# Kernel tuning notes

Measured on AMD Instinct MI355X. Metric: run time of the kernel, lower is better.

## Reference

```python
import jax, jax.numpy as jnp
import numpy as np

B, S, D, H = 1, 4096, 1024, 16
DH = D // H

def setup_inputs() -> dict:
    key = jax.random.key(0)
    ks = jax.random.split(key, 5)
    std = float(np.sqrt(2.0 / (D + D)))
    return {
        "x": jax.random.normal(ks[0], (B, S, D), dtype=jnp.float32),
        "Wq": jax.random.normal(ks[1], (D, D), dtype=jnp.float32) * std,
        "Wk": jax.random.normal(ks[2], (D, D), dtype=jnp.float32) * std,
        "Wv": jax.random.normal(ks[3], (D, D), dtype=jnp.float32) * std,
        "Wo": jax.random.normal(ks[4], (D, D), dtype=jnp.float32) * std,
    }

def reference(x, Wq, Wk, Wv, Wo):
    # projections: input @ W.T, then split heads: b s (h d) -> b h s d
    def split_heads(t):
        b, s, _ = t.shape
        return t.reshape(b, s, H, DH).transpose(0, 2, 1, 3)
    q = split_heads(x @ Wq.T)
    k = split_heads(x @ Wk.T)
    v = split_heads(x @ Wv.T)
    scale = 1.0 / jnp.sqrt(jnp.asarray(DH, dtype=x.dtype))
    scores = jnp.einsum("bhqd,bhkd->bhqk", q, k) * scale  # (b,h,s,s)
    # causal mask: allow k <= q
    causal = jnp.tril(jnp.ones((S, S), dtype=bool))
    scores = jnp.where(causal, scores, jnp.finfo(scores.dtype).min)
    attn = jax.nn.softmax(scores, axis=-1)
    out = jnp.einsum("bhqk,bhkd->bhqd", attn, v)  # (b,h,s,d)
    out = out.transpose(0, 2, 1, 3).reshape(B, S, D)  # b h s d -> b s (h d)
    return out @ Wo.T
```

## Files before the change

### kernel.cpp

```cpp
#include <hip/hip_runtime.h>
#include <math.h>

#define SEQ 4096
#define DM  1024
#define NH  16
#define DH  64

typedef _Float16 h16;
typedef __attribute__((ext_vector_type(4))) _Float16 h16x4;
typedef __attribute__((ext_vector_type(8))) _Float16 h16x8;
typedef __attribute__((ext_vector_type(4))) float f32x4;

__device__ __forceinline__ void gload_lds16(const h16* g, h16* l) {
    __builtin_amdgcn_global_load_lds(
        (const __attribute__((address_space(1))) void*)g,
        (__attribute__((address_space(3))) void*)l, 16, 0, 0);
}

__global__ __launch_bounds__(256) void cvt_all(const float* __restrict__ x,
                                               const float* __restrict__ wq,
                                               const float* __restrict__ wk,
                                               const float* __restrict__ wv,
                                               const float* __restrict__ wo,
                                               h16* __restrict__ dst) {
    const size_t SD4 = (size_t)SEQ * DM / 4;
    const size_t DD4 = (size_t)DM * DM / 4;
    const size_t i = (size_t)blockIdx.x * 256 + threadIdx.x;
    const float* src;
    size_t off;
    if (i < SD4) { src = x; off = i; }
    else {
        const size_t j = i - SD4;
        const int wsel = (int)(j >> 18);
        off = j & (DD4 - 1);
        src = (wsel == 0) ? wq : (wsel == 1) ? wk : (wsel == 2) ? wv : wo;
    }
    const float4 v = ((const float4*)src)[off];
    h16x4 o = { (h16)v.x, (h16)v.y, (h16)v.z, (h16)v.w };
    ((h16x4*)dst)[i] = o;
}

#define GT 32

__global__ __launch_bounds__(256) void gemm_qkv(const h16* __restrict__ xh,
                                                const h16* __restrict__ Wq,
                                                const h16* __restrict__ Wk,
                                                const h16* __restrict__ Wv,
                                                h16* __restrict__ Qh,
                                                h16* __restrict__ Kh,
                                                h16* __restrict__ Vth,
                                                float scl) {
    __shared__ h16 As[2][128 * GT];
    __shared__ h16 Bs[2][128 * GT];

    const int z    = blockIdx.z;
    const h16* B   = (z == 0) ? Wq : (z == 1) ? Wk : Wv;
    const int t    = threadIdx.x;
    const int lane = t & 63;
    const int w    = t >> 6;
    const int wm   = (w >> 1) * 64;
    const int wn   = (w & 1) * 64;
    const int l15  = lane & 15;
    const int lq   = lane >> 4;
    const int lq8  = lq * 8;
    const int m0   = blockIdx.y * 128;
    const int n0   = blockIdx.x * 128;
    const int K = DM, M = SEQ, N = DM;

    const int srow = w * 16 + (lane >> 2);
    const int scol = (lane & 3) * 8;
    const h16* pa0 = xh + (size_t)(m0 + srow) * K + scol;
    const h16* pa1 = xh + (size_t)(m0 + 64 + srow) * K + scol;
    const h16* pb0 = B  + (size_t)(n0 + srow) * K + scol;
    const h16* pb1 = B  + (size_t)(n0 + 64 + srow) * K + scol;

    f32x4 acc[4][4] = {};

    for (int k0 = 0; k0 < K; k0 += 64) {
        __syncthreads();
        #pragma unroll
        for (int s = 0; s < 2; ++s) {
            const int ko = k0 + s * 32;
            gload_lds16(pa0 + ko, &As[s][w * 512]);
            gload_lds16(pa1 + ko, &As[s][2048 + w * 512]);
            gload_lds16(pb0 + ko, &Bs[s][w * 512]);
            gload_lds16(pb1 + ko, &Bs[s][2048 + w * 512]);
        }
        __syncthreads();

        #pragma unroll
        for (int s = 0; s < 2; ++s) {
            h16x8 af[4], bf[4];
            #pragma unroll
            for (int i = 0; i < 4; ++i)
                af[i] = *(const h16x8*)&As[s][(wm + i * 16 + l15) * GT + lq8];
            #pragma unroll
            for (int j = 0; j < 4; ++j)
                bf[j] = *(const h16x8*)&Bs[s][(wn + j * 16 + l15) * GT + lq8];
            #pragma unroll
            for (int i = 0; i < 4; ++i)
                #pragma unroll
                for (int j = 0; j < 4; ++j)
                    acc[i][j] = __builtin_amdgcn_mfma_f32_16x16x32_f16(af[i], bf[j], acc[i][j], 0, 0, 0);
        }
    }

    const int cr = wm + lq * 4;
    const int cc = wn + l15;
    if (z == 2) {
        #pragma unroll
        for (int i = 0; i < 4; ++i)
            #pragma unroll
            for (int j = 0; j < 4; ++j) {
                const int gm0 = m0 + cr + i * 16;
                const int gn  = n0 + cc + j * 16;
                h16x4 v = { (h16)acc[i][j][0], (h16)acc[i][j][1],
                            (h16)acc[i][j][2], (h16)acc[i][j][3] };
                *(h16x4*)(Vth + (size_t)gn * M + gm0) = v;
            }
    } else {
        h16* Og = (z == 0) ? Qh : Kh;
        const float e = (z == 0) ? scl : 1.0f;
        #pragma unroll
        for (int i = 0; i < 4; ++i)
            #pragma unroll
            for (int j = 0; j < 4; ++j)
                #pragma unroll
                for (int r = 0; r < 4; ++r) {
                    const int gm = m0 + cr + i * 16 + r;
                    const int gn = n0 + cc + j * 16;
                    Og[(size_t)gm * N + gn] = (h16)(acc[i][j][r] * e);
                }
    }
}

__global__ __launch_bounds__(256) void gemm_out(const h16* __restrict__ A,
                                                const h16* __restrict__ B,
                                                float* __restrict__ C) {
    __shared__ h16 As[2][128 * GT];
    __shared__ h16 Bs[2][128 * GT];

    const int t    = threadIdx.x;
    const int lane = t & 63;
    const int w    = t >> 6;
    const int wm   = (w >> 1) * 64;
    const int wn   = (w & 1) * 64;
    const int l15  = lane & 15;
    const int lq   = lane >> 4;
    const int lq8  = lq * 8;
    const int m0   = blockIdx.y * 128;
    const int n0   = blockIdx.x * 128;
    const int K = DM, N = DM;

    const int srow = w * 16 + (lane >> 2);
    const int scol = (lane & 3) * 8;
    const h16* pa0 = A + (size_t)(m0 + srow) * K + scol;
    const h16* pa1 = A + (size_t)(m0 + 64 + srow) * K + scol;
    const h16* pb0 = B + (size_t)(n0 + srow) * K + scol;
    const h16* pb1 = B + (size_t)(n0 + 64 + srow) * K + scol;

    f32x4 acc[4][4] = {};

    for (int k0 = 0; k0 < K; k0 += 64) {
        __syncthreads();
        #pragma unroll
        for (int s = 0; s < 2; ++s) {
            const int ko = k0 + s * 32;
            gload_lds16(pa0 + ko, &As[s][w * 512]);
            gload_lds16(pa1 + ko, &As[s][2048 + w * 512]);
            gload_lds16(pb0 + ko, &Bs[s][w * 512]);
            gload_lds16(pb1 + ko, &Bs[s][2048 + w * 512]);
        }
        __syncthreads();

        #pragma unroll
        for (int s = 0; s < 2; ++s) {
            h16x8 af[4], bf[4];
            #pragma unroll
            for (int i = 0; i < 4; ++i)
                af[i] = *(const h16x8*)&As[s][(wm + i * 16 + l15) * GT + lq8];
            #pragma unroll
            for (int j = 0; j < 4; ++j)
                bf[j] = *(const h16x8*)&Bs[s][(wn + j * 16 + l15) * GT + lq8];
            #pragma unroll
            for (int i = 0; i < 4; ++i)
                #pragma unroll
                for (int j = 0; j < 4; ++j)
                    acc[i][j] = __builtin_amdgcn_mfma_f32_16x16x32_f16(af[i], bf[j], acc[i][j], 0, 0, 0);
        }
    }

    const int cr = wm + lq * 4;
    const int cc = wn + l15;
    #pragma unroll
    for (int i = 0; i < 4; ++i)
        #pragma unroll
        for (int j = 0; j < 4; ++j)
            #pragma unroll
            for (int r = 0; r < 4; ++r)
                C[(size_t)(m0 + cr + i * 16 + r) * N + n0 + cc + j * 16] = acc[i][j][r];
}

#define AST 80

__global__ __launch_bounds__(256, 3) void flash_attn_mfma(
        const h16* __restrict__ Qg, const h16* __restrict__ Kg,
        const h16* __restrict__ Vt, h16* __restrict__ Og) {
    __shared__ h16 Ks[64 * AST];
    __shared__ h16 Vs[64 * AST];
    __shared__ h16 Ps[64 * AST];

    const int qt   = 63 - (int)blockIdx.y;
    const int hh   = blockIdx.x;
    const int t    = threadIdx.x;
    const int lane = t & 63;
    const int w    = t >> 6;
    const int l15  = lane & 15;
    const int lq   = lane >> 4;
    const int lq8  = lq * 8;
    const int hc   = hh * DH;
    const int q0   = qt * 64;
    const int q_loc = w * 16 + l15;

    const int r1 = t >> 3;
    const int r2 = r1 + 32;
    const int c1 = (t & 7) * 8;

    *(h16x8*)&Ks[r1 * AST + c1] = *(const h16x8*)(Qg + (size_t)(q0 + r1) * DM + hc + c1);
    *(h16x8*)&Ks[r2 * AST + c1] = *(const h16x8*)(Qg + (size_t)(q0 + r2) * DM + hc + c1);

    h16x8 kv1 = *(const h16x8*)(Kg + (size_t)(r1) * DM + hc + c1);
    h16x8 kv2 = *(const h16x8*)(Kg + (size_t)(r2) * DM + hc + c1);
    h16x8 vv1 = *(const h16x8*)(Vt + (size_t)(hc + r1) * SEQ + c1);
    h16x8 vv2 = *(const h16x8*)(Vt + (size_t)(hc + r2) * SEQ + c1);

    __syncthreads();
    h16x8 qf[2];
    qf[0] = *(const h16x8*)&Ks[q_loc * AST + lq8];
    qf[1] = *(const h16x8*)&Ks[q_loc * AST + 32 + lq8];

    float m_st = -1e30f, l_st = 0.0f;
    f32x4 o[4] = {};
    h16* const ps = &Ps[(size_t)q_loc * AST];

    for (int kt = 0; kt <= qt; ++kt) {
        __syncthreads();
        *(h16x8*)&Ks[r1 * AST + c1] = kv1;
        *(h16x8*)&Ks[r2 * AST + c1] = kv2;
        *(h16x8*)&Vs[r1 * AST + c1] = vv1;
        *(h16x8*)&Vs[r2 * AST + c1] = vv2;
        __syncthreads();
        if (kt < qt) {
            const int k0n = (kt + 1) * 64;
            kv1 = *(const h16x8*)(Kg + (size_t)(k0n + r1) * DM + hc + c1);
            kv2 = *(const h16x8*)(Kg + (size_t)(k0n + r2) * DM + hc + c1);
            vv1 = *(const h16x8*)(Vt + (size_t)(hc + r1) * SEQ + k0n + c1);
            vv2 = *(const h16x8*)(Vt + (size_t)(hc + r2) * SEQ + k0n + c1);
        }

        f32x4 s[4] = {};
        #pragma unroll
        for (int kc = 0; kc < 2; ++kc)
            #pragma unroll
            for (int jj = 0; jj < 4; ++jj) {
                const h16x8 kf = *(const h16x8*)&Ks[(jj * 16 + l15) * AST + kc * 32 + lq8];
                s[jj] = __builtin_amdgcn_mfma_f32_16x16x32_f16(kf, qf[kc], s[jj], 0, 0, 0);
            }

        if (kt == qt) {
            #pragma unroll
            for (int jj = 0; jj < 4; ++jj)
                #pragma unroll
                for (int r = 0; r < 4; ++r)
                    if ((jj * 16 + lq * 4 + r) > q_loc) s[jj][r] = -1e30f;
        }
        float mx = m_st;
        #pragma unroll
        for (int jj = 0; jj < 4; ++jj)
            #pragma unroll
            for (int r = 0; r < 4; ++r)
                mx = fmaxf(mx, s[jj][r]);
        mx = fmaxf(mx, __shfl_xor(mx, 16, 64));
        mx = fmaxf(mx, __shfl_xor(mx, 32, 64));
        const float alpha = exp2f(m_st - mx);
        m_st = mx;
        float sum = 0.0f;
        #pragma unroll
        for (int jj = 0; jj < 4; ++jj) {
            const float p0 = exp2f(s[jj][0] - mx);
            const float p1 = exp2f(s[jj][1] - mx);
            const float p2 = exp2f(s[jj][2] - mx);
            const float p3 = exp2f(s[jj][3] - mx);
            sum += (p0 + p1) + (p2 + p3);
            h16x4 pk = { (h16)p0, (h16)p1, (h16)p2, (h16)p3 };
            *(h16x4*)(ps + jj * 16 + lq * 4) = pk;
        }
        sum += __shfl_xor(sum, 16, 64);
        sum += __shfl_xor(sum, 32, 64);
        l_st = l_st * alpha + sum;
        #pragma unroll
        for (int jj = 0; jj < 4; ++jj)
            #pragma unroll
            for (int r = 0; r < 4; ++r)
                o[jj][r] *= alpha;

        asm volatile("s_waitcnt lgkmcnt(0)" ::: "memory");
        h16x8 pf[2];
        pf[0] = *(const h16x8*)(ps + lq8);
        pf[1] = *(const h16x8*)(ps + 32 + lq8);

        #pragma unroll
        for (int kc = 0; kc < 2; ++kc)
            #pragma unroll
            for (int jj = 0; jj < 4; ++jj) {
                const h16x8 vf = *(const h16x8*)&Vs[(jj * 16 + l15) * AST + kc * 32 + lq8];
                o[jj] = __builtin_amdgcn_mfma_f32_16x16x32_f16(vf, pf[kc], o[jj], 0, 0, 0);
            }
    }

    const float il = 1.0f / l_st;
    const size_t qg = (size_t)(q0 + q_loc) * DM + hc;
    #pragma unroll
    for (int jj = 0; jj < 4; ++jj) {
        h16x4 ov = { (h16)(o[jj][0] * il), (h16)(o[jj][1] * il),
                     (h16)(o[jj][2] * il), (h16)(o[jj][3] * il) };
        *(h16x4*)(Og + qg + jj * 16 + lq * 4) = ov;
    }
}

extern "C" void kernel_launch(void* const* d_in, const int* in_sizes, int n_in,
                              void* d_out, int out_size, void* d_ws, size_t ws_size,
                              hipStream_t stream) {
    const float* x  = (const float*)d_in[0];
    const float* Wq = (const float*)d_in[1];
    const float* Wk = (const float*)d_in[2];
    const float* Wv = (const float*)d_in[3];
    const float* Wo = (const float*)d_in[4];
    float* out = (float*)d_out;

    const size_t SD = (size_t)SEQ * DM;
    const size_t DD = (size_t)DM * DM;

    h16* xh  = (h16*)d_ws;
    h16* wqh = xh + SD;
    h16* wkh = wqh + DD;
    h16* wvh = wkh + DD;
    h16* woh = wvh + DD;
    h16* Qh  = woh + DD;
    h16* Kh  = Qh + SD;
    h16* Vth = Kh + SD;
    h16* AOh = Vth + SD;

    const dim3 blk(256);

    cvt_all<<<(int)((SD + 4 * DD) / 4 / 256), blk, 0, stream>>>(x, Wq, Wk, Wv, Wo, xh);

    const float SCL = 0.125f * 1.44269504088896340736f;

    gemm_qkv<<<dim3(DM / 128, SEQ / 128, 3), blk, 0, stream>>>(
        xh, wqh, wkh, wvh, Qh, Kh, Vth, SCL);

    flash_attn_mfma<<<dim3(NH, 64), blk, 0, stream>>>(Qh, Kh, Vth, AOh);

    gemm_out<<<dim3(DM / 128, SEQ / 128), blk, 0, stream>>>(AOh, woh, out);
}
```

Measured before the change: 233.4 us.

## Load K/V fragments directly into registers in attention; shrink output GEMM M tile

```diff
diff --git a/kernel.cpp b/kernel.cpp
--- a/kernel.cpp
+++ b/kernel.cpp
@@ -137,29 +137,28 @@
 __global__ __launch_bounds__(256) void gemm_out(const h16* __restrict__ A,
                                                 const h16* __restrict__ B,
                                                 float* __restrict__ C) {
-    __shared__ h16 As[2][128 * GT];
+    __shared__ h16 As[2][64 * GT];
     __shared__ h16 Bs[2][128 * GT];
 
     const int t    = threadIdx.x;
     const int lane = t & 63;
     const int w    = t >> 6;
-    const int wm   = (w >> 1) * 64;
+    const int wm   = (w >> 1) * 32;
     const int wn   = (w & 1) * 64;
     const int l15  = lane & 15;
     const int lq   = lane >> 4;
     const int lq8  = lq * 8;
-    const int m0   = blockIdx.y * 128;
+    const int m0   = blockIdx.y * 64;
     const int n0   = blockIdx.x * 128;
     const int K = DM, N = DM;
 
     const int srow = w * 16 + (lane >> 2);
     const int scol = (lane & 3) * 8;
     const h16* pa0 = A + (size_t)(m0 + srow) * K + scol;
-    const h16* pa1 = A + (size_t)(m0 + 64 + srow) * K + scol;
     const h16* pb0 = B + (size_t)(n0 + srow) * K + scol;
     const h16* pb1 = B + (size_t)(n0 + 64 + srow) * K + scol;
 
-    f32x4 acc[4][4] = {};
+    f32x4 acc[2][4] = {};
 
     for (int k0 = 0; k0 < K; k0 += 64) {
         __syncthreads();
@@ -167,7 +166,6 @@
         for (int s = 0; s < 2; ++s) {
             const int ko = k0 + s * 32;
             gload_lds16(pa0 + ko, &As[s][w * 512]);
-            gload_lds16(pa1 + ko, &As[s][2048 + w * 512]);
             gload_lds16(pb0 + ko, &Bs[s][w * 512]);
             gload_lds16(pb1 + ko, &Bs[s][2048 + w * 512]);
         }
@@ -175,15 +173,15 @@
 
         #pragma unroll
         for (int s = 0; s < 2; ++s) {
-            h16x8 af[4], bf[4];
-            #pragma unroll
-            for (int i = 0; i < 4; ++i)
+            h16x8 af[2], bf[4];
+            #pragma unroll
+            for (int i = 0; i < 2; ++i)
                 af[i] = *(const h16x8*)&As[s][(wm + i * 16 + l15) * GT + lq8];
             #pragma unroll
             for (int j = 0; j < 4; ++j)
                 bf[j] = *(const h16x8*)&Bs[s][(wn + j * 16 + l15) * GT + lq8];
             #pragma unroll
-            for (int i = 0; i < 4; ++i)
+            for (int i = 0; i < 2; ++i)
                 #pragma unroll
                 for (int j = 0; j < 4; ++j)
                     acc[i][j] = __builtin_amdgcn_mfma_f32_16x16x32_f16(af[i], bf[j], acc[i][j], 0, 0, 0);
@@ -193,7 +191,7 @@
     const int cr = wm + lq * 4;
     const int cc = wn + l15;
     #pragma unroll
-    for (int i = 0; i < 4; ++i)
+    for (int i = 0; i < 2; ++i)
         #pragma unroll
         for (int j = 0; j < 4; ++j)
             #pragma unroll
@@ -201,14 +199,12 @@
                 C[(size_t)(m0 + cr + i * 16 + r) * N + n0 + cc + j * 16] = acc[i][j][r];
 }
 
-#define AST 80
-
-__global__ __launch_bounds__(256, 3) void flash_attn_mfma(
+#define PST 72
+
+__global__ __launch_bounds__(256, 2) void flash_attn_mfma(
         const h16* __restrict__ Qg, const h16* __restrict__ Kg,
         const h16* __restrict__ Vt, h16* __restrict__ Og) {
-    __shared__ h16 Ks[64 * AST];
-    __shared__ h16 Vs[64 * AST];
-    __shared__ h16 Ps[64 * AST];
+    __shared__ h16 Ps[64 * PST];
 
     const int qt   = 63 - (int)blockIdx.y;
     const int hh   = blockIdx.x;
@@ -222,50 +218,41 @@
     const int q0   = qt * 64;
     const int q_loc = w * 16 + l15;
 
-    const int r1 = t >> 3;
-    const int r2 = r1 + 32;
-    const int c1 = (t & 7) * 8;
-
-    *(h16x8*)&Ks[r1 * AST + c1] = *(const h16x8*)(Qg + (size_t)(q0 + r1) * DM + hc + c1);
-    *(h16x8*)&Ks[r2 * AST + c1] = *(const h16x8*)(Qg + (size_t)(q0 + r2) * DM + hc + c1);
-
-    h16x8 kv1 = *(const h16x8*)(Kg + (size_t)(r1) * DM + hc + c1);
-    h16x8 kv2 = *(const h16x8*)(Kg + (size_t)(r2) * DM + hc + c1);
-    h16x8 vv1 = *(const h16x8*)(Vt + (size_t)(hc + r1) * SEQ + c1);
-    h16x8 vv2 = *(const h16x8*)(Vt + (size_t)(hc + r2) * SEQ + c1);
-
-    __syncthreads();
-    h16x8 qf[2];
-    qf[0] = *(const h16x8*)&Ks[q_loc * AST + lq8];
-    qf[1] = *(const h16x8*)&Ks[q_loc * AST + 32 + lq8];
+    const h16* qp = Qg + (size_t)(q0 + q_loc) * DM + hc + lq8;
+    h16x8 qf[2] = { *(const h16x8*)qp, *(const h16x8*)(qp + 32) };
+
+    const h16* kbase = Kg + (size_t)l15 * DM + hc + lq8;
+    const h16* vbase = Vt + (size_t)(hc + l15) * SEQ + lq8;
+
+    h16x8 kf[2][4], vf[2][4];
+    #pragma unroll
+    for (int kc = 0; kc < 2; ++kc)
+        #pragma unroll
+        for (int jj = 0; jj < 4; ++jj) {
+            kf[kc][jj] = *(const h16x8*)(kbase + (size_t)(jj * 16) * DM + kc * 32);
+            vf[kc][jj] = *(const h16x8*)(vbase + (size_t)(jj * 16) * SEQ + kc * 32);
+        }
 
     float m_st = -1e30f, l_st = 0.0f;
     f32x4 o[4] = {};
-    h16* const ps = &Ps[(size_t)q_loc * AST];
+    h16* const ps = &Ps[(size_t)q_loc * PST];
 
     for (int kt = 0; kt <= qt; ++kt) {
-        __syncthreads();
-        *(h16x8*)&Ks[r1 * AST + c1] = kv1;
-        *(h16x8*)&Ks[r2 * AST + c1] = kv2;
-        *(h16x8*)&Vs[r1 * AST + c1] = vv1;
-        *(h16x8*)&Vs[r2 * AST + c1] = vv2;
-        __syncthreads();
+        f32x4 s[4] = {};
+        #pragma unroll
+        for (int kc = 0; kc < 2; ++kc)
+            #pragma unroll
+            for (int jj = 0; jj < 4; ++jj)
+                s[jj] = __builtin_amdgcn_mfma_f32_16x16x32_f16(kf[kc][jj], qf[kc], s[jj], 0, 0, 0);
+
         if (kt < qt) {
             const int k0n = (kt + 1) * 64;
-            kv1 = *(const h16x8*)(Kg + (size_t)(k0n + r1) * DM + hc + c1);
-            kv2 = *(const h16x8*)(Kg + (size_t)(k0n + r2) * DM + hc + c1);
-            vv1 = *(const h16x8*)(Vt + (size_t)(hc + r1) * SEQ + k0n + c1);
-            vv2 = *(const h16x8*)(Vt + (size_t)(hc + r2) * SEQ + k0n + c1);
-        }
-
-        f32x4 s[4] = {};
-        #pragma unroll
-        for (int kc = 0; kc < 2; ++kc)
-            #pragma unroll
-            for (int jj = 0; jj < 4; ++jj) {
-                const h16x8 kf = *(const h16x8*)&Ks[(jj * 16 + l15) * AST + kc * 32 + lq8];
-                s[jj] = __builtin_amdgcn_mfma_f32_16x16x32_f16(kf, qf[kc], s[jj], 0, 0, 0);
-            }
+            #pragma unroll
+            for (int kc = 0; kc < 2; ++kc)
+                #pragma unroll
+                for (int jj = 0; jj < 4; ++jj)
+                    kf[kc][jj] = *(const h16x8*)(kbase + (size_t)(k0n + jj * 16) * DM + kc * 32);
+        }
 
         if (kt == qt) {
             #pragma unroll
@@ -312,10 +299,17 @@
         #pragma unroll
         for (int kc = 0; kc < 2; ++kc)
             #pragma unroll
-            for (int jj = 0; jj < 4; ++jj) {
-                const h16x8 vf = *(const h16x8*)&Vs[(jj * 16 + l15) * AST + kc * 32 + lq8];
-                o[jj] = __builtin_amdgcn_mfma_f32_16x16x32_f16(vf, pf[kc], o[jj], 0, 0, 0);
-            }
+            for (int jj = 0; jj < 4; ++jj)
+                o[jj] = __builtin_amdgcn_mfma_f32_16x16x32_f16(vf[kc][jj], pf[kc], o[jj], 0, 0, 0);
+
+        if (kt < qt) {
+            const int k0n = (kt + 1) * 64;
+            #pragma unroll
+            for (int kc = 0; kc < 2; ++kc)
+                #pragma unroll
+                for (int jj = 0; jj < 4; ++jj)
+                    vf[kc][jj] = *(const h16x8*)(vbase + (size_t)(jj * 16) * SEQ + k0n + kc * 32);
+        }
     }
 
     const float il = 1.0f / l_st;
@@ -362,5 +356,5 @@
 
     flash_attn_mfma<<<dim3(NH, 64), blk, 0, stream>>>(Qh, Kh, Vth, AOh);
 
-    gemm_out<<<dim3(DM / 128, SEQ / 128), blk, 0, stream>>>(AOh, woh, out);
-}
+    gemm_out<<<dim3(DM / 128, SEQ / 64), blk, 0, stream>>>(AOh, woh, out);
+}
```

Measured after the change: 388.8 us. 1.67x slower.

## Split causal attention over KV chunks with a combine pass; shrink out-projection M tile

Applied to the files above, without the earlier changes.

```diff
diff --git a/kernel.cpp b/kernel.cpp
--- a/kernel.cpp
+++ b/kernel.cpp
@@ -5,6 +5,7 @@
 #define DM  1024
 #define NH  16
 #define DH  64
+#define NS  4
 
 typedef _Float16 h16;
 typedef __attribute__((ext_vector_type(4))) _Float16 h16x4;
@@ -137,29 +138,28 @@
 __global__ __launch_bounds__(256) void gemm_out(const h16* __restrict__ A,
                                                 const h16* __restrict__ B,
                                                 float* __restrict__ C) {
-    __shared__ h16 As[2][128 * GT];
+    __shared__ h16 As[2][64 * GT];
     __shared__ h16 Bs[2][128 * GT];
 
     const int t    = threadIdx.x;
     const int lane = t & 63;
     const int w    = t >> 6;
-    const int wm   = (w >> 1) * 64;
+    const int wm   = (w >> 1) * 32;
     const int wn   = (w & 1) * 64;
     const int l15  = lane & 15;
     const int lq   = lane >> 4;
     const int lq8  = lq * 8;
-    const int m0   = blockIdx.y * 128;
+    const int m0   = blockIdx.y * 64;
     const int n0   = blockIdx.x * 128;
     const int K = DM, N = DM;
 
     const int srow = w * 16 + (lane >> 2);
     const int scol = (lane & 3) * 8;
     const h16* pa0 = A + (size_t)(m0 + srow) * K + scol;
-    const h16* pa1 = A + (size_t)(m0 + 64 + srow) * K + scol;
     const h16* pb0 = B + (size_t)(n0 + srow) * K + scol;
     const h16* pb1 = B + (size_t)(n0 + 64 + srow) * K + scol;
 
-    f32x4 acc[4][4] = {};
+    f32x4 acc[2][4] = {};
 
     for (int k0 = 0; k0 < K; k0 += 64) {
         __syncthreads();
@@ -167,7 +167,6 @@
         for (int s = 0; s < 2; ++s) {
             const int ko = k0 + s * 32;
             gload_lds16(pa0 + ko, &As[s][w * 512]);
-            gload_lds16(pa1 + ko, &As[s][2048 + w * 512]);
             gload_lds16(pb0 + ko, &Bs[s][w * 512]);
             gload_lds16(pb1 + ko, &Bs[s][2048 + w * 512]);
         }
@@ -175,15 +174,15 @@
 
         #pragma unroll
         for (int s = 0; s < 2; ++s) {
-            h16x8 af[4], bf[4];
-            #pragma unroll
-            for (int i = 0; i < 4; ++i)
+            h16x8 af[2], bf[4];
+            #pragma unroll
+            for (int i = 0; i < 2; ++i)
                 af[i] = *(const h16x8*)&As[s][(wm + i * 16 + l15) * GT + lq8];
             #pragma unroll
             for (int j = 0; j < 4; ++j)
                 bf[j] = *(const h16x8*)&Bs[s][(wn + j * 16 + l15) * GT + lq8];
             #pragma unroll
-            for (int i = 0; i < 4; ++i)
+            for (int i = 0; i < 2; ++i)
                 #pragma unroll
                 for (int j = 0; j < 4; ++j)
                     acc[i][j] = __builtin_amdgcn_mfma_f32_16x16x32_f16(af[i], bf[j], acc[i][j], 0, 0, 0);
@@ -193,7 +192,7 @@
     const int cr = wm + lq * 4;
     const int cc = wn + l15;
     #pragma unroll
-    for (int i = 0; i < 4; ++i)
+    for (int i = 0; i < 2; ++i)
         #pragma unroll
         for (int j = 0; j < 4; ++j)
             #pragma unroll
@@ -203,15 +202,17 @@
 
 #define AST 80
 
-__global__ __launch_bounds__(256, 3) void flash_attn_mfma(
+__global__ __launch_bounds__(256, 3) void flash_attn_split(
         const h16* __restrict__ Qg, const h16* __restrict__ Kg,
-        const h16* __restrict__ Vt, h16* __restrict__ Og) {
+        const h16* __restrict__ Vt, h16* __restrict__ OP,
+        float* __restrict__ Mb, float* __restrict__ Lb) {
     __shared__ h16 Ks[64 * AST];
     __shared__ h16 Vs[64 * AST];
     __shared__ h16 Ps[64 * AST];
 
     const int qt   = 63 - (int)blockIdx.y;
     const int hh   = blockIdx.x;
+    const int sp   = blockIdx.z;
     const int t    = threadIdx.x;
     const int lane = t & 63;
     const int w    = t >> 6;
@@ -222,6 +223,11 @@
     const int q0   = qt * 64;
     const int q_loc = w * 16 + l15;
 
+    const int ntile = qt + 1;
+    const int chunk = (ntile + NS - 1) / NS;
+    const int kts   = sp * chunk;
+    const int kte   = (kts + chunk < ntile) ? (kts + chunk) : ntile;
+
     const int r1 = t >> 3;
     const int r2 = r1 + 32;
     const int c1 = (t & 7) * 8;
@@ -229,10 +235,11 @@
     *(h16x8*)&Ks[r1 * AST + c1] = *(const h16x8*)(Qg + (size_t)(q0 + r1) * DM + hc + c1);
     *(h16x8*)&Ks[r2 * AST + c1] = *(const h16x8*)(Qg + (size_t)(q0 + r2) * DM + hc + c1);
 
-    h16x8 kv1 = *(const h16x8*)(Kg + (size_t)(r1) * DM + hc + c1);
-    h16x8 kv2 = *(const h16x8*)(Kg + (size_t)(r2) * DM + hc + c1);
-    h16x8 vv1 = *(const h16x8*)(Vt + (size_t)(hc + r1) * SEQ + c1);
-    h16x8 vv2 = *(const h16x8*)(Vt + (size_t)(hc + r2) * SEQ + c1);
+    const int kb0 = kts * 64;
+    h16x8 kv1 = *(const h16x8*)(Kg + (size_t)(kb0 + r1) * DM + hc + c1);
+    h16x8 kv2 = *(const h16x8*)(Kg + (size_t)(kb0 + r2) * DM + hc + c1);
+    h16x8 vv1 = *(const h16x8*)(Vt + (size_t)(hc + r1) * SEQ + kb0 + c1);
+    h16x8 vv2 = *(const h16x8*)(Vt + (size_t)(hc + r2) * SEQ + kb0 + c1);
 
     __syncthreads();
     h16x8 qf[2];
@@ -243,14 +250,14 @@
     f32x4 o[4] = {};
     h16* const ps = &Ps[(size_t)q_loc * AST];
 
-    for (int kt = 0; kt <= qt; ++kt) {
+    for (int kt = kts; kt < kte; ++kt) {
         __syncthreads();
         *(h16x8*)&Ks[r1 * AST + c1] = kv1;
         *(h16x8*)&Ks[r2 * AST + c1] = kv2;
         *(h16x8*)&Vs[r1 * AST + c1] = vv1;
         *(h16x8*)&Vs[r2 * AST + c1] = vv2;
         __syncthreads();
-        if (kt < qt) {
+        if (kt + 1 < kte) {
             const int k0n = (kt + 1) * 64;
             kv1 = *(const h16x8*)(Kg + (size_t)(k0n + r1) * DM + hc + c1);
             kv2 = *(const h16x8*)(Kg + (size_t)(k0n + r2) * DM + hc + c1);
@@ -318,14 +325,54 @@
             }
     }
 
-    const float il = 1.0f / l_st;
+    h16* const op = OP + (size_t)sp * SEQ * DM;
     const size_t qg = (size_t)(q0 + q_loc) * DM + hc;
     #pragma unroll
     for (int jj = 0; jj < 4; ++jj) {
-        h16x4 ov = { (h16)(o[jj][0] * il), (h16)(o[jj][1] * il),
-                     (h16)(o[jj][2] * il), (h16)(o[jj][3] * il) };
-        *(h16x4*)(Og + qg + jj * 16 + lq * 4) = ov;
-    }
+        h16x4 ov = { (h16)o[jj][0], (h16)o[jj][1], (h16)o[jj][2], (h16)o[jj][3] };
+        *(h16x4*)(op + qg + jj * 16 + lq * 4) = ov;
+    }
+    if (lq == 0) {
+        const size_t mi = ((size_t)sp * NH + hh) * SEQ + q0 + q_loc;
+        Mb[mi] = m_st;
+        Lb[mi] = l_st;
+    }
+}
+
+__global__ __launch_bounds__(256) void combine(const h16* __restrict__ OP,
+                                               const float* __restrict__ Mb,
+                                               const float* __restrict__ Lb,
+                                               h16* __restrict__ AOh) {
+    const int i  = blockIdx.x * 256 + threadIdx.x;
+    const int q  = i >> 8;
+    const int c4 = (i & 255) * 4;
+    const int hh = c4 >> 6;
+
+    float ms[NS], ls[NS];
+    float mstar = -1e30f;
+    #pragma unroll
+    for (int s = 0; s < NS; ++s) {
+        const size_t mi = ((size_t)s * NH + hh) * SEQ + q;
+        ms[s] = Mb[mi];
+        ls[s] = Lb[mi];
+        mstar = fmaxf(mstar, ms[s]);
+    }
+    float L = 0.0f;
+    float acc[4] = {};
+    #pragma unroll
+    for (int s = 0; s < NS; ++s) {
+        const float ws = exp2f(ms[s] - mstar);
+        L += ls[s] * ws;
+        const h16x4 ov = *(const h16x4*)(OP + (size_t)s * SEQ * DM + (size_t)q * DM + c4);
+        acc[0] += ws * (float)ov[0];
+        acc[1] += ws * (float)ov[1];
+        acc[2] += ws * (float)ov[2];
+        acc[3] += ws * (float)ov[3];
+    }
+    const float inv = 1.0f / L;
+    h16x4 r = { (h16)(acc[0] * inv), (h16)(acc[1] * inv),
+                (h16)(acc[2] * inv), (h16)(acc[3] * inv) };
+    *(h16x4*)(AOh + (size_t)q * DM + c4) = r;
 }
 
 extern "C" void kernel_launch(void* const* d_in, const int* in_sizes, int n_in,
@@ -350,6 +397,9 @@
     h16* Kh  = Qh + SD;
     h16* Vth = Kh + SD;
     h16* AOh = Vth + SD;
+    h16* OP  = AOh + SD;
+    float* Mb = (float*)(OP + (size_t)NS * SD);
+    float* Lb = Mb + (size_t)NS * NH * SEQ;
 
     const dim3 blk(256);
 
@@ -360,7 +410,9 @@
     gemm_qkv<<<dim3(DM / 128, SEQ / 128, 3), blk, 0, stream>>>(
         xh, wqh, wkh, wvh, Qh, Kh, Vth, SCL);
 
-    flash_attn_mfma<<<dim3(NH, 64), blk, 0, stream>>>(Qh, Kh, Vth, AOh);
-
-    gemm_out<<<dim3(DM / 128, SEQ / 128), blk, 0, stream>>>(AOh, woh, out);
-}
+    flash_attn_split<<<dim3(NH, 64, NS), blk, 0, stream>>>(Qh, Kh, Vth, OP, Mb, Lb);
+
+    combine<<<(int)(SD / 4 / 256), blk, 0, stream>>>(OP, Mb, Lb, AOh);
+
+    gemm_out<<<dim3(DM / 128, SEQ / 64), blk, 0, stream>>>(AOh, woh, out);
+}
```

New measurement: 223.9 us. 4.1% less time.
